# Performance work log

Hardware: AMD Instinct MI355X
Metric: run time of the kernel (lower is better)

The kernel has to match this reference:

```python
import jax, jax.numpy as jnp
import numpy as np

MASK_SUB = 1000000.0  # the module subtracts 1e6 from masked scores (not -inf)

def setup_inputs() -> dict:
    key = jax.random.key(0)
    kq, kk, kv = jax.random.split(key, 3)
    B, S, D = 16, 2048, 64
    q = jax.random.normal(kq, (B, S, D), dtype=jnp.float32)
    k = jax.random.normal(kk, (B, S, D), dtype=jnp.float32)
    v = jax.random.normal(kv, (B, S, D), dtype=jnp.float32)
    return {"q": q, "k": k, "v": v}

def reference(q, k, v):
    d_k = k.shape[-1]
    s = k.shape[-2]
    # scores: [b, s_q, s_k]
    scores = jnp.einsum('bqd,bkd->bqk', q, k) / jnp.sqrt(jnp.asarray(d_k, q.dtype))
    # causal mask: strictly-upper-triangular entries get 1e6 subtracted (matches torch.triu diagonal=1)
    causal = jnp.triu(jnp.ones((s, s), dtype=bool), k=1)
    scores = jnp.where(causal[None, :, :], scores - MASK_SUB, scores)
    weights = jax.nn.softmax(scores, axis=-1)
    return jnp.einsum('bqk,bkd->bqd', weights, v)
```

## Files before the change

### kernel.cpp

```cpp
#include <hip/hip_runtime.h>
#include <stdint.h>


typedef __bf16 bf16x8 __attribute__((ext_vector_type(8)));
typedef float f32x4 __attribute__((ext_vector_type(4)));
typedef float f32x16 __attribute__((ext_vector_type(16)));

#define NB 16
#define SL 2048
#define DH 64
#define NCH 8

__device__ __forceinline__ __bf16 f2bf(float f) {
    uint32_t u = __builtin_bit_cast(uint32_t, f);
    u += 0x7FFFu + ((u >> 16) & 1u);
    uint16_t h = (uint16_t)(u >> 16);
    return __builtin_bit_cast(__bf16, h);
}

__device__ __forceinline__ void load_lds16(const void* g, void* l) {
    __builtin_amdgcn_global_load_lds(
        (const __attribute__((address_space(1))) uint32_t*)g,
        (__attribute__((address_space(3))) uint32_t*)l, 16, 0, 0);
}

__global__ __launch_bounds__(256) void prepass(
        const float* __restrict__ K, const float* __restrict__ V,
        __bf16* __restrict__ Kb, __bf16* __restrict__ Vt) {
    __shared__ float tl[64][68];
    const int b    = blockIdx.x >> 5;
    const int tile = blockIdx.x & 31;
    const int s0   = tile << 6;
    const int t    = threadIdx.x;
    const int r    = t >> 2;
    const int c0   = (t & 3) * 16;

    const float* Kp = K + ((size_t)(b * SL + s0) + r) * DH + c0;
    float4 f0 = ((const float4*)Kp)[0], f1 = ((const float4*)Kp)[1];
    float4 f2 = ((const float4*)Kp)[2], f3 = ((const float4*)Kp)[3];
    bf16x8 w0, w1;
    w0[0]=f2bf(f0.x); w0[1]=f2bf(f0.y); w0[2]=f2bf(f0.z); w0[3]=f2bf(f0.w);
    w0[4]=f2bf(f1.x); w0[5]=f2bf(f1.y); w0[6]=f2bf(f1.z); w0[7]=f2bf(f1.w);
    w1[0]=f2bf(f2.x); w1[1]=f2bf(f2.y); w1[2]=f2bf(f2.z); w1[3]=f2bf(f2.w);
    w1[4]=f2bf(f3.x); w1[5]=f2bf(f3.y); w1[6]=f2bf(f3.z); w1[7]=f2bf(f3.w);
    __bf16* Kbp = Kb + ((size_t)(b * SL + s0) + r) * DH;
    const int j0 = c0 >> 3;
    *(bf16x8*)(Kbp + ((j0       ^ (r & 7)) * 8)) = w0;
    *(bf16x8*)(Kbp + (((j0 + 1) ^ (r & 7)) * 8)) = w1;

    const float* Vp = V + ((size_t)(b * SL + s0) + r) * DH + c0;
    ((float4*)&tl[r][c0])[0] = ((const float4*)Vp)[0];
    ((float4*)&tl[r][c0])[1] = ((const float4*)Vp)[1];
    ((float4*)&tl[r][c0])[2] = ((const float4*)Vp)[2];
    ((float4*)&tl[r][c0])[3] = ((const float4*)Vp)[3];
    __syncthreads();

    __bf16* img = Vt + ((size_t)(b * 32 + tile)) * 4096;
#pragma unroll
    for (int half = 0; half < 2; ++half) {
        const int c = half * 256 + t;
        const int d = c >> 3, slot = c & 7;
        const int jj = slot ^ (d & 7);
        bf16x8 w;
#pragma unroll
        for (int e = 0; e < 8; ++e) w[e] = f2bf(tl[jj * 8 + e][d]);
        *(bf16x8*)(img + c * 8) = w;
    }
}

__global__ __launch_bounds__(256, 3) void attn_fwd(
        const float* __restrict__ Q, const __bf16* __restrict__ Kb,
        const __bf16* __restrict__ Vt, float* __restrict__ part,
        float* __restrict__ lpart) {
    __shared__ __align__(16) __bf16 lK[2][4096];
    __shared__ __align__(16) __bf16 lV[2][4096];
    __shared__ __align__(16) __bf16 lP[4][2048];

    const int bid = blockIdx.x;
    const int b   = bid & 15;
    const int jr  = 71 - (bid >> 4);
    int Kp_ = 0;
    while ((Kp_ + 1) * (Kp_ + 2) <= jr) ++Kp_;
    const int d_  = jr - Kp_ * (Kp_ + 1);
    const int u   = 2 * Kp_ + (d_ & 1);
    const int c   = d_ >> 1;
    const int kt0   = c * 4;
    const int ktmax = min(kt0 + 4, 2 * u + 2);

    const int tid  = threadIdx.x;
    const int wave = tid >> 6, lane = tid & 63;
    const int col  = lane & 31, h = lane >> 5;
    const int xk   = col & 7;
    const int Tw   = 2 * u + (wave >> 1);
    const int qglob = Tw * 64 + (wave & 1) * 32 + col;

    bf16x8 qf[4];
    const float* qp = Q + ((size_t)b * SL + qglob) * DH;
#pragma unroll
    for (int s = 0; s < 4; ++s) {
        const float* base = qp + s * 16 + h * 8;
        float4 a0 = ((const float4*)base)[0];
        float4 a1 = ((const float4*)base)[1];
        qf[s][0] = f2bf(a0.x * 0.125f); qf[s][1] = f2bf(a0.y * 0.125f);
        qf[s][2] = f2bf(a0.z * 0.125f); qf[s][3] = f2bf(a0.w * 0.125f);
        qf[s][4] = f2bf(a1.x * 0.125f); qf[s][5] = f2bf(a1.y * 0.125f);
        qf[s][6] = f2bf(a1.z * 0.125f); qf[s][7] = f2bf(a1.w * 0.125f);
    }

    f32x16 acc[2];
    acc[0] = (f32x16)0.0f; acc[1] = (f32x16)0.0f;
    float accl = 0.0f;

    const __bf16* Kbase = Kb + (size_t)b * SL * DH;
    const __bf16* Vbase = Vt + (size_t)b * 32 * 4096;
    __bf16* lPw = lP[wave];

    auto stage = [&](int kt2) {
        const int bufi = kt2 & 1;
        const __bf16* Ks = Kbase + (size_t)kt2 * 4096;
        const __bf16* Vs = Vbase + (size_t)kt2 * 4096;
#pragma unroll
        for (int i2 = 0; i2 < 2; ++i2) {
            load_lds16(Ks + (size_t)(i2 * 256 + tid) * 8,
                       &lK[bufi][(i2 * 256 + wave * 64) * 8]);
            load_lds16(Vs + (size_t)(i2 * 256 + tid) * 8,
                       &lV[bufi][(i2 * 256 + wave * 64) * 8]);
        }
    };

    stage(kt0);
    for (int kt = kt0; kt < ktmax; ++kt) {
        __syncthreads();
        if (kt + 1 < ktmax) stage(kt + 1);
        if (kt > Tw) continue;
        const __bf16* K_ = lK[kt & 1];
        const __bf16* V_ = lV[kt & 1];

#pragma unroll
        for (int mt = 0; mt < 2; ++mt) {
            f32x16 sc = (f32x16)0.0f;
            const int key = mt * 32 + col;
#pragma unroll
            for (int s = 0; s < 4; ++s) {
                bf16x8 kf = *(const bf16x8*)&K_[key * 64 + (((2 * s + h) ^ xk) << 3)];
                sc = __builtin_amdgcn_mfma_f32_32x32x16_bf16(kf, qf[s], sc, 0, 0, 0);
            }
            if (kt == Tw) {
                const int kb = kt * 64 + mt * 32 + 4 * h;
#pragma unroll
                for (int g = 0; g < 4; ++g)
#pragma unroll
                    for (int r = 0; r < 4; ++r)
                        if (kb + 8 * g + r > qglob) sc[4 * g + r] = -1.0e30f;
            }
#pragma unroll
            for (int g = 0; g < 4; ++g) {
                float p0 = __expf(sc[4 * g + 0]), p1 = __expf(sc[4 * g + 1]);
                float p2 = __expf(sc[4 * g + 2]), p3 = __expf(sc[4 * g + 3]);
                accl += (p0 + p1) + (p2 + p3);
                uint32_t u0 = __builtin_amdgcn_perm(__builtin_bit_cast(uint32_t, p1),
                                                   __builtin_bit_cast(uint32_t, p0), 0x07060302u);
                uint32_t u1 = __builtin_amdgcn_perm(__builtin_bit_cast(uint32_t, p3),
                                                   __builtin_bit_cast(uint32_t, p2), 0x07060302u);
                uint2 val; val.x = u0; val.y = u1;
                *(uint2*)&lPw[(mt * 4 + g) * 256 + col * 8 + 4 * h] = val;
            }
        }
        asm volatile("" ::: "memory");

#pragma unroll
        for (int s = 0; s < 4; ++s) {
            bf16x8 pf = *(const bf16x8*)&lPw[(2 * s + h) * 256 + col * 8];
#pragma unroll
            for (int mt = 0; mt < 2; ++mt) {
                const int dd = mt * 32 + col;
                bf16x8 vf = *(const bf16x8*)&V_[dd * 64 + (((2 * s + h) ^ xk) << 3)];
                acc[mt] = __builtin_amdgcn_mfma_f32_32x32x16_bf16(vf, pf, acc[mt], 0, 0, 0);
            }
        }
    }

    float* pp = part + ((size_t)(b * SL + qglob) * NCH + c) * DH;
#pragma unroll
    for (int mt = 0; mt < 2; ++mt)
#pragma unroll
        for (int g = 0; g < 4; ++g) {
            float4 o4;
            o4.x = acc[mt][4 * g + 0]; o4.y = acc[mt][4 * g + 1];
            o4.z = acc[mt][4 * g + 2]; o4.w = acc[mt][4 * g + 3];
            *(float4*)(pp + mt * 32 + 8 * g + 4 * h) = o4;
        }
    const float lsum = accl + __shfl_xor(accl, 32);
    if (h == 0)
        lpart[(size_t)(b * SL + qglob) * NCH + c] = lsum;
}

__global__ __launch_bounds__(256) void combine(
        const float* __restrict__ part, const float* __restrict__ lpart,
        float* __restrict__ O) {
    const int tid = threadIdx.x;
    const int r   = blockIdx.x * 16 + (tid >> 4);
    const int d4  = tid & 15;
    const int T   = (r >> 6) & 31;
    const int nch = (T + 4) >> 2;
    float4 s = make_float4(0.f, 0.f, 0.f, 0.f);
    float ls = 0.f;
    for (int c = 0; c < nch; ++c) {
        float4 p = *(const float4*)(part + ((size_t)r * NCH + c) * DH + d4 * 4);
        s.x += p.x; s.y += p.y; s.z += p.z; s.w += p.w;
        ls += lpart[(size_t)r * NCH + c];
    }
    const float inv = 1.0f / ls;
    float4 o; o.x = s.x * inv; o.y = s.y * inv; o.z = s.z * inv; o.w = s.w * inv;
    *(float4*)(O + (size_t)r * DH + d4 * 4) = o;
}

extern "C" void kernel_launch(void* const* d_in, const int* in_sizes, int n_in,
                              void* d_out, int out_size, void* d_ws, size_t ws_size,
                              hipStream_t stream) {
    const float* q = (const float*)d_in[0];
    const float* k = (const float*)d_in[1];
    const float* v = (const float*)d_in[2];
    float* o = (float*)d_out;
    __bf16* Kb = (__bf16*)d_ws;
    __bf16* Vt = Kb + (size_t)NB * SL * DH;
    float*  pt = (float*)((char*)d_ws + (8u << 20));
    float*  lp = pt + (size_t)NB * SL * NCH * DH;
    hipLaunchKernelGGL(prepass, dim3(NB * 32), dim3(256), 0, stream, k, v, Kb, Vt);
    hipLaunchKernelGGL(attn_fwd, dim3(NB * 72), dim3(256), 0, stream, q, Kb, Vt, pt, lp);
    hipLaunchKernelGGL(combine, dim3(NB * SL / 16), dim3(256), 0, stream, pt, lp, o);
}
```

Baseline: 101.9 us.

## Load K/V fragments directly from global memory per wave, drop LDS staging

Removes the double-buffered LDS staging of K and V tiles, and the XOR swizzle in the prepass, so each wave reads its MFMA fragments straight from global memory into registers. Work is now assigned per wave rather than per block, with each wave owning its own 32-query, 4-key-tile chunk, which removes the block-level barriers and the idle waves that skipped tiles beyond their diagonal. The cost is repeated global/L2 traffic for K and V across waves that used to share one LDS tile, no prefetch overlap, and higher register pressure from holding 16 K/V fragments at once.

```diff
diff --git a/kernel.cpp b/kernel.cpp
--- a/kernel.cpp
+++ b/kernel.cpp
@@ -3,7 +3,6 @@
 
 
 typedef __bf16 bf16x8 __attribute__((ext_vector_type(8)));
-typedef float f32x4 __attribute__((ext_vector_type(4)));
 typedef float f32x16 __attribute__((ext_vector_type(16)));
 
 #define NB 16
@@ -16,12 +15,6 @@
     u += 0x7FFFu + ((u >> 16) & 1u);
     uint16_t h = (uint16_t)(u >> 16);
     return __builtin_bit_cast(__bf16, h);
-}
-
-__device__ __forceinline__ void load_lds16(const void* g, void* l) {
-    __builtin_amdgcn_global_load_lds(
-        (const __attribute__((address_space(1))) uint32_t*)g,
-        (__attribute__((address_space(3))) uint32_t*)l, 16, 0, 0);
 }
 
 __global__ __launch_bounds__(256) void prepass(
@@ -43,10 +36,9 @@
     w0[4]=f2bf(f1.x); w0[5]=f2bf(f1.y); w0[6]=f2bf(f1.z); w0[7]=f2bf(f1.w);
     w1[0]=f2bf(f2.x); w1[1]=f2bf(f2.y); w1[2]=f2bf(f2.z); w1[3]=f2bf(f2.w);
     w1[4]=f2bf(f3.x); w1[5]=f2bf(f3.y); w1[6]=f2bf(f3.z); w1[7]=f2bf(f3.w);
-    __bf16* Kbp = Kb + ((size_t)(b * SL + s0) + r) * DH;
-    const int j0 = c0 >> 3;
-    *(bf16x8*)(Kbp + ((j0       ^ (r & 7)) * 8)) = w0;
-    *(bf16x8*)(Kbp + (((j0 + 1) ^ (r & 7)) * 8)) = w1;
+    __bf16* Kbp = Kb + ((size_t)(b * SL + s0) + r) * DH + c0;
+    *(bf16x8*)(Kbp)     = w0;
+    *(bf16x8*)(Kbp + 8) = w1;
 
     const float* Vp = V + ((size_t)(b * SL + s0) + r) * DH + c0;
     ((float4*)&tl[r][c0])[0] = ((const float4*)Vp)[0];
@@ -60,10 +52,9 @@
     for (int half = 0; half < 2; ++half) {
         const int c = half * 256 + t;
         const int d = c >> 3, slot = c & 7;
-        const int jj = slot ^ (d & 7);
         bf16x8 w;
 #pragma unroll
-        for (int e = 0; e < 8; ++e) w[e] = f2bf(tl[jj * 8 + e][d]);
+        for (int e = 0; e < 8; ++e) w[e] = f2bf(tl[slot * 8 + e][d]);
         *(bf16x8*)(img + c * 8) = w;
     }
 }
@@ -72,27 +63,26 @@
         const float* __restrict__ Q, const __bf16* __restrict__ Kb,
         const __bf16* __restrict__ Vt, float* __restrict__ part,
         float* __restrict__ lpart) {
-    __shared__ __align__(16) __bf16 lK[2][4096];
-    __shared__ __align__(16) __bf16 lV[2][4096];
     __shared__ __align__(16) __bf16 lP[4][2048];
-
-    const int bid = blockIdx.x;
-    const int b   = bid & 15;
-    const int jr  = 71 - (bid >> 4);
-    int Kp_ = 0;
-    while ((Kp_ + 1) * (Kp_ + 2) <= jr) ++Kp_;
-    const int d_  = jr - Kp_ * (Kp_ + 1);
-    const int u   = 2 * Kp_ + (d_ & 1);
-    const int c   = d_ >> 1;
-    const int kt0   = c * 4;
-    const int ktmax = min(kt0 + 4, 2 * u + 2);
 
     const int tid  = threadIdx.x;
     const int wave = tid >> 6, lane = tid & 63;
     const int col  = lane & 31, h = lane >> 5;
-    const int xk   = col & 7;
-    const int Tw   = 2 * u + (wave >> 1);
-    const int qglob = Tw * 64 + (wave & 1) * 32 + col;
+
+    const int b   = blockIdx.x & 15;
+    const int jjw = (blockIdx.x >> 4) * 4 + wave;
+    const int jr  = 287 - jjw;
+    const int half = jr & 1;
+    const int idx  = jr >> 1;
+    int k = 0;
+    while (2 * (k + 1) * (k + 2) <= idx) ++k;
+    const int off = idx - 2 * k * (k + 1);
+    const int q_  = off / (k + 1);
+    const int c   = off - q_ * (k + 1);
+    const int T   = 4 * k + q_;
+    const int kt0   = 4 * c;
+    const int ktmax = min(kt0 + 4, T + 1);
+    const int qglob = T * 64 + half * 32 + col;
 
     bf16x8 qf[4];
     const float* qp = Q + ((size_t)b * SL + qglob) * DH;
@@ -115,37 +105,29 @@
     const __bf16* Vbase = Vt + (size_t)b * 32 * 4096;
     __bf16* lPw = lP[wave];
 
-    auto stage = [&](int kt2) {
-        const int bufi = kt2 & 1;
-        const __bf16* Ks = Kbase + (size_t)kt2 * 4096;
-        const __bf16* Vs = Vbase + (size_t)kt2 * 4096;
-#pragma unroll
-        for (int i2 = 0; i2 < 2; ++i2) {
-            load_lds16(Ks + (size_t)(i2 * 256 + tid) * 8,
-                       &lK[bufi][(i2 * 256 + wave * 64) * 8]);
-            load_lds16(Vs + (size_t)(i2 * 256 + tid) * 8,
-                       &lV[bufi][(i2 * 256 + wave * 64) * 8]);
-        }
-    };
-
-    stage(kt0);
     for (int kt = kt0; kt < ktmax; ++kt) {
-        __syncthreads();
-        if (kt + 1 < ktmax) stage(kt + 1);
-        if (kt > Tw) continue;
-        const __bf16* K_ = lK[kt & 1];
-        const __bf16* V_ = lV[kt & 1];
+        const __bf16* K_ = Kbase + (size_t)kt * 4096;
+        const __bf16* V_ = Vbase + (size_t)kt * 4096;
+
+        bf16x8 kf[2][4], vf[2][4];
+#pragma unroll
+        for (int mt = 0; mt < 2; ++mt)
+#pragma unroll
+            for (int s = 0; s < 4; ++s)
+                kf[mt][s] = *(const bf16x8*)&K_[(mt * 32 + col) * 64 + s * 16 + h * 8];
+#pragma unroll
+        for (int mt = 0; mt < 2; ++mt)
+#pragma unroll
+            for (int s = 0; s < 4; ++s)
+                vf[mt][s] = *(const bf16x8*)&V_[(mt * 32 + col) * 64 + s * 16 + h * 8];
 
 #pragma unroll
         for (int mt = 0; mt < 2; ++mt) {
             f32x16 sc = (f32x16)0.0f;
-            const int key = mt * 32 + col;
-#pragma unroll
-            for (int s = 0; s < 4; ++s) {
-                bf16x8 kf = *(const bf16x8*)&K_[key * 64 + (((2 * s + h) ^ xk) << 3)];
-                sc = __builtin_amdgcn_mfma_f32_32x32x16_bf16(kf, qf[s], sc, 0, 0, 0);
-            }
-            if (kt == Tw) {
+#pragma unroll
+            for (int s = 0; s < 4; ++s)
+                sc = __builtin_amdgcn_mfma_f32_32x32x16_bf16(kf[mt][s], qf[s], sc, 0, 0, 0);
+            if (kt == T) {
                 const int kb = kt * 64 + mt * 32 + 4 * h;
 #pragma unroll
                 for (int g = 0; g < 4; ++g)
@@ -172,11 +154,8 @@
         for (int s = 0; s < 4; ++s) {
             bf16x8 pf = *(const bf16x8*)&lPw[(2 * s + h) * 256 + col * 8];
 #pragma unroll
-            for (int mt = 0; mt < 2; ++mt) {
-                const int dd = mt * 32 + col;
-                bf16x8 vf = *(const bf16x8*)&V_[dd * 64 + (((2 * s + h) ^ xk) << 3)];
-                acc[mt] = __builtin_amdgcn_mfma_f32_32x32x16_bf16(vf, pf, acc[mt], 0, 0, 0);
-            }
+            for (int mt = 0; mt < 2; ++mt)
+                acc[mt] = __builtin_amdgcn_mfma_f32_32x32x16_bf16(vf[mt][s], pf, acc[mt], 0, 0, 0);
         }
     }
 
@@ -227,6 +206,6 @@
     float*  pt = (float*)((char*)d_ws + (8u << 20));
     float*  lp = pt + (size_t)NB * SL * NCH * DH;
     hipLaunchKernelGGL(prepass, dim3(NB * 32), dim3(256), 0, stream, k, v, Kb, Vt);
-    hipLaunchKernelGGL(attn_fwd, dim3(NB * 72), dim3(256), 0, stream, q, Kb, Vt, pt, lp);
+    hipLaunchKernelGGL(attn_fwd, dim3(1152), dim3(256), 0, stream, q, Kb, Vt, pt, lp);
     hipLaunchKernelGGL(combine, dim3(NB * SL / 16), dim3(256), 0, stream, pt, lp, o);
 }
```

Measured after the change: 126.5 us. 24.1% more time.
